# Kernel optimization log

Hardware: AMD Instinct MI355X
Metric: run time of the kernel (lower is better)

The kernel has to match this reference:

```python
import jax, jax.numpy as jnp
import numpy as np

N_NODES = 20000
N_PATHS = 100000
D_IN = 128
H = 128
N_GRAPHS = 128
N_CLASSES = 10
EPS = 1e-5


def _bn(x, g, b):
    # BatchNorm1d in training mode: biased batch statistics
    m = x.mean(0)
    v = x.var(0)
    return g * (x - m) * jax.lax.rsqrt(v + EPS) + b


def _lstm_final_h(seq, w_ih, w_hh, b_ih, b_hh):
    # seq: [N, T, H] -> final hidden state [N, H]; torch gate order i,f,g,o
    N = seq.shape[0]
    Hd = w_hh.shape[1]
    xg = jnp.einsum('nti,gi->ntg', seq, w_ih) + b_ih + b_hh  # [N, T, 4H]

    def step(carry, g_t):
        h, c = carry
        g = g_t + h @ w_hh.T
        i, f, gg, o = jnp.split(g, 4, axis=-1)
        c = jax.nn.sigmoid(f) * c + jax.nn.sigmoid(i) * jnp.tanh(gg)
        h = jax.nn.sigmoid(o) * jnp.tanh(c)
        return (h, c), None

    init = (jnp.zeros((N, Hd), seq.dtype), jnp.zeros((N, Hd), seq.dtype))
    (h, _), _ = jax.lax.scan(step, init, jnp.swapaxes(xg, 0, 1))
    return h


def setup_inputs() -> dict:
    key = jax.random.key(0)
    ks = jax.random.split(key, 24)
    s = 0.05
    inp = {
        'x': jax.random.normal(ks[0], (N_NODES, D_IN), jnp.float32),
        'path_2': jax.random.randint(ks[1], (N_PATHS, 2), 0, N_NODES),
        'path_3': jax.random.randint(ks[2], (N_PATHS, 3), 0, N_NODES),
        'batch': jnp.sort(jax.random.randint(ks[3], (N_NODES,), 0, N_GRAPHS)),
        # feature encoder: Linear -> BN -> ReLU -> Linear -> BN -> ReLU
        'fe_w1': jax.random.normal(ks[4], (H, D_IN)) * s,
        'fe_b1': jnp.zeros((H,)),
        'fe_g1': jnp.ones((H,)),
        'fe_be1': jnp.zeros((H,)),
        'fe_w2': jax.random.normal(ks[5], (H, H)) * s,
        'fe_b2': jnp.zeros((H,)),
        'fe_g2': jnp.ones((H,)),
        'fe_be2': jnp.zeros((H,)),
        # shared single-layer LSTM (input H -> hidden H)
        'w_ih': jax.random.normal(ks[6], (4 * H, H)) * s,
        'w_hh': jax.random.normal(ks[7], (4 * H, H)) * s,
        'b_ih': jnp.zeros((4 * H,)),
        'b_hh': jnp.zeros((4 * H,)),
        # per-conv batch norms (cutoff-1 = 2 layers)
        'bn1_g': jnp.ones((H,)),
        'bn1_b': jnp.zeros((H,)),
        'bn2_g': jnp.ones((H,)),
        'bn2_b': jnp.zeros((H,)),
        # readout
        'lin1_w': jax.random.normal(ks[8], (H, H)) * s,
        'lin1_b': jnp.zeros((H,)),
        'lin2_w': jax.random.normal(ks[9], (N_CLASSES, H)) * s,
        'lin2_b': jnp.zeros((N_CLASSES,)),
    }
    return inp


def reference(x, path_2, path_3, batch,
              fe_w1, fe_b1, fe_g1, fe_be1, fe_w2, fe_b2, fe_g2, fe_be2,
              w_ih, w_hh, b_ih, b_hh,
              bn1_g, bn1_b, bn2_g, bn2_b,
              lin1_w, lin1_b, lin2_w, lin2_b):
    # feature encoder
    h = jax.nn.relu(_bn(x @ fe_w1.T + fe_b1, fe_g1, fe_be1))
    h = jax.nn.relu(_bn(h @ fe_w2.T + fe_b2, fe_g2, fe_be2))
    # PathConv layers: gather paths -> shared LSTM -> scatter-add -> residual+BN+ReLU
    for paths, bg, bb in ((path_2, bn1_g, bn1_b), (path_3, bn2_g, bn2_b)):
        seq = h[paths]                                   # [n_paths, T, H]
        hf = _lstm_final_h(seq, w_ih, w_hh, b_ih, b_hh)  # [n_paths, H]
        agg = jax.ops.segment_sum(hf, paths[:, -1], num_segments=h.shape[0])
        h = jax.nn.relu(_bn(agg + h, bg, bb))
    # global add pool + MLP head
    pooled = jax.ops.segment_sum(h, batch, num_segments=N_GRAPHS)
    out = jax.nn.relu(pooled @ lin1_w.T + lin1_b)
    return out @ lin2_w.T + lin2_b
```

## Files before the change

kernel.cpp:

```cpp
#include <hip/hip_runtime.h>
#include <cmath>

#define NN 20000
#define NP 100000
#define D  128
#define G4 512
#define NG 128
#define NC 10
#define CHUNK 20000

__device__ __forceinline__ float sigf(float x) { return 1.0f / (1.0f + expf(-x)); }

__device__ __forceinline__ void stage_chunk(
    const float* __restrict__ A, const float* __restrict__ W,
    float4* As4, float4* Ws4, int bm, int bn, int M, int N,
    int koff, int sr, int sc)
{
#pragma unroll
  for (int pass = 0; pass < 8; ++pass) {
    int r = pass * 16 + sr;
    int sw = sc ^ ((r >> 3) & 7);
    int ga = bm + r; ga = ga < M ? ga : M - 1;
    As4[r * 16 + sw] = *(const float4*)(A + (size_t)ga * 128 + koff + sc * 4);
    int gw = bn + r; gw = gw < N ? gw : N - 1;
    Ws4[r * 16 + sw] = *(const float4*)(W + (size_t)gw * 128 + koff + sc * 4);
  }
}

__device__ __forceinline__ void compute_chunk(
    const float4* As4, const float4* Ws4,
    int tm, int tn, int axor, int wxor, float acc[8][8])
{
#pragma unroll 2
  for (int k4 = 0; k4 < 16; ++k4) {
    float4 av[8], wv[8];
#pragma unroll
    for (int i = 0; i < 8; ++i) av[i] = As4[(tm + i) * 16 + (k4 ^ axor)];
#pragma unroll
    for (int j = 0; j < 8; ++j) wv[j] = Ws4[(tn + j) * 16 + (k4 ^ wxor)];
#pragma unroll
    for (int i = 0; i < 8; ++i)
#pragma unroll
      for (int j = 0; j < 8; ++j) {
        acc[i][j] = fmaf(av[i].x, wv[j].x, acc[i][j]);
        acc[i][j] = fmaf(av[i].y, wv[j].y, acc[i][j]);
        acc[i][j] = fmaf(av[i].z, wv[j].z, acc[i][j]);
        acc[i][j] = fmaf(av[i].w, wv[j].w, acc[i][j]);
      }
  }
}

__global__ __launch_bounds__(256) void gemm128(
    const float* __restrict__ A, const float* __restrict__ W,
    const float* __restrict__ bias, float* __restrict__ C,
    int M, int N, int relu)
{
  __shared__ float4 As4[2048];
  __shared__ float4 Ws4[2048];

  const int tid = threadIdx.x;
  const int bm = blockIdx.x * 128;
  const int bn = blockIdx.y * 128;

  const int ty = tid >> 4, tx = tid & 15;
  const int tm = ty * 8, tn = tx * 8;
  const int axor = ty & 7, wxor = tx & 7;
  const int sr = tid >> 4, sc = tid & 15;

  float acc[8][8] = {};

  stage_chunk(A, W, As4, Ws4, bm, bn, M, N, 0, sr, sc);
  __syncthreads();
  compute_chunk(As4, Ws4, tm, tn, axor, wxor, acc);
  __syncthreads();
  stage_chunk(A, W, As4, Ws4, bm, bn, M, N, 64, sr, sc);
  __syncthreads();
  compute_chunk(As4, Ws4, tm, tn, axor, wxor, acc);

#pragma unroll
  for (int i = 0; i < 8; ++i) {
    int r = bm + tm + i;
    if (r >= M) continue;
    int cbase = bn + tn;
    if (cbase + 7 < N && ((((size_t)r * N + cbase) & 3) == 0)) {
#pragma unroll
      for (int jj = 0; jj < 2; ++jj) {
        float4 v;
        v.x = acc[i][jj * 4 + 0] + (bias ? bias[cbase + jj * 4 + 0] : 0.f);
        v.y = acc[i][jj * 4 + 1] + (bias ? bias[cbase + jj * 4 + 1] : 0.f);
        v.z = acc[i][jj * 4 + 2] + (bias ? bias[cbase + jj * 4 + 2] : 0.f);
        v.w = acc[i][jj * 4 + 3] + (bias ? bias[cbase + jj * 4 + 3] : 0.f);
        if (relu) { v.x = fmaxf(v.x, 0.f); v.y = fmaxf(v.y, 0.f);
                    v.z = fmaxf(v.z, 0.f); v.w = fmaxf(v.w, 0.f); }
        *(float4*)(C + (size_t)r * N + cbase + jj * 4) = v;
      }
    } else {
#pragma unroll
      for (int j = 0; j < 8; ++j) {
        int cn = cbase + j;
        if (cn >= N) continue;
        float v = acc[i][j] + (bias ? bias[cn] : 0.f);
        if (relu) v = fmaxf(v, 0.f);
        C[(size_t)r * N + cn] = v;
      }
    }
  }
}

__global__ void zero_kernel(float* p, int n) {
  for (int i = blockIdx.x * blockDim.x + threadIdx.x; i < n; i += gridDim.x * blockDim.x)
    p[i] = 0.f;
}

__global__ void zero_int(int* p, int n) {
  for (int i = blockIdx.x * blockDim.x + threadIdx.x; i < n; i += gridDim.x * blockDim.x)
    p[i] = 0;
}

__global__ void addvec_kernel(const float* a, const float* b, float* o, int n) {
  int i = blockIdx.x * blockDim.x + threadIdx.x;
  if (i < n) o[i] = a[i] + b[i];
}

__global__ __launch_bounds__(256) void bn_stats(const float* __restrict__ u,
                                                float* __restrict__ stats,
                                                int M, int rowsPerBlock) {
  __shared__ float sh[512];
  const int j = threadIdx.x & 127;
  const int half = threadIdx.x >> 7;
  int r0 = blockIdx.x * rowsPerBlock;
  int r1 = min(M, r0 + rowsPerBlock);
  float s = 0.f, q = 0.f;
  for (int r = r0 + half; r < r1; r += 2) {
    float v = u[(size_t)r * 128 + j];
    s += v; q += v * v;
  }
  sh[threadIdx.x] = s;
  sh[256 + threadIdx.x] = q;
  __syncthreads();
  if (threadIdx.x < 128) {
    atomicAdd(&stats[j], sh[j] + sh[j + 128]);
    atomicAdd(&stats[128 + j], sh[256 + j] + sh[256 + j + 128]);
  }
}

__global__ void bn_apply_relu(const float* __restrict__ u, const float* __restrict__ stats,
                              const float* __restrict__ g, const float* __restrict__ b,
                              float* __restrict__ out, int n4, float invM) {
  int idx = blockIdx.x * blockDim.x + threadIdx.x;
  if (idx >= n4) return;
  int q = idx & 31;
  float4 uv = ((const float4*)u)[idx];
  float4 sv = ((const float4*)stats)[q];
  float4 qv = ((const float4*)stats)[32 + q];
  float4 gv = ((const float4*)g)[q];
  float4 bv = ((const float4*)b)[q];
  float4 o;
  { float m = sv.x * invM, var = qv.x * invM - m * m;
    o.x = fmaxf(gv.x * (uv.x - m) * rsqrtf(var + 1e-5f) + bv.x, 0.f); }
  { float m = sv.y * invM, var = qv.y * invM - m * m;
    o.y = fmaxf(gv.y * (uv.y - m) * rsqrtf(var + 1e-5f) + bv.y, 0.f); }
  { float m = sv.z * invM, var = qv.z * invM - m * m;
    o.z = fmaxf(gv.z * (uv.z - m) * rsqrtf(var + 1e-5f) + bv.z, 0.f); }
  { float m = sv.w * invM, var = qv.w * invM - m * m;
    o.w = fmaxf(gv.w * (uv.w - m) * rsqrtf(var + 1e-5f) + bv.w, 0.f); }
  ((float4*)out)[idx] = o;
}

__global__ void hist_k(const int* __restrict__ path, int stride, int col, int np,
                       int* __restrict__ cnt) {
  int i = blockIdx.x * blockDim.x + threadIdx.x;
  if (i < np) atomicAdd(&cnt[path[(size_t)i * stride + col]], 1);
}

__global__ __launch_bounds__(256) void scan_bins(const int* __restrict__ cnt,
                                                 int* __restrict__ rp) {
  __shared__ int sh[256];
  const int t = threadIdx.x;
  const int SEG = (NN + 255) / 256;
  int lo = t * SEG, hi = min(NN, lo + SEG);
  int s = 0;
  for (int i = lo; i < hi; ++i) s += cnt[i];
  sh[t] = s;
  __syncthreads();
  for (int off = 1; off < 256; off <<= 1) {
    int v = (t >= off) ? sh[t - off] : 0;
    __syncthreads();
    sh[t] += v;
    __syncthreads();
  }
  int base = (t == 0) ? 0 : sh[t - 1];
  for (int i = lo; i < hi; ++i) { rp[i] = base; base += cnt[i]; }
  if (t == 0) rp[NN] = sh[255];
}

__global__ void scatter_k(const int* __restrict__ path, int stride, int col, int np,
                          const int* __restrict__ rp, int* __restrict__ cur,
                          int* __restrict__ perm) {
  int i = blockIdx.x * blockDim.x + threadIdx.x;
  if (i < np) {
    int b = path[(size_t)i * stride + col];
    int pos = atomicAdd(&cur[b], 1);
    perm[rp[b] + pos] = i;
  }
}

__global__ void lstm_step0(const float* __restrict__ Z, float* __restrict__ H1,
                           float* __restrict__ C1, int n4) {
  int idx = blockIdx.x * blockDim.x + threadIdx.x;
  if (idx >= n4) return;
  int v = idx >> 5, q = idx & 31;
  const float4* z = (const float4*)(Z + (size_t)v * G4);
  float4 zi = z[q], zg = z[64 + q], zo = z[96 + q];
  float4 c, h;
  c.x = sigf(zi.x) * tanhf(zg.x); h.x = sigf(zo.x) * tanhf(c.x);
  c.y = sigf(zi.y) * tanhf(zg.y); h.y = sigf(zo.y) * tanhf(c.y);
  c.z = sigf(zi.z) * tanhf(zg.z); h.z = sigf(zo.z) * tanhf(c.z);
  c.w = sigf(zi.w) * tanhf(zg.w); h.w = sigf(zo.w) * tanhf(c.w);
  ((float4*)C1)[idx] = c;
  ((float4*)H1)[idx] = h;
}

__device__ __forceinline__ void lstm_gate4(const float4 zi, const float4 zf,
                                           const float4 zg, const float4 zo,
                                           const float4 ri, const float4 rf,
                                           const float4 rg, const float4 ro,
                                           const float4 cin, float4* cout, float4* hout) {
  float c, out;
  c = sigf(zf.x + rf.x) * cin.x + sigf(zi.x + ri.x) * tanhf(zg.x + rg.x);
  out = sigf(zo.x + ro.x) * tanhf(c); cout->x = c; hout->x = out;
  c = sigf(zf.y + rf.y) * cin.y + sigf(zi.y + ri.y) * tanhf(zg.y + rg.y);
  out = sigf(zo.y + ro.y) * tanhf(c); cout->y = c; hout->y = out;
  c = sigf(zf.z + rf.z) * cin.z + sigf(zi.z + ri.z) * tanhf(zg.z + rg.z);
  out = sigf(zo.z + ro.z) * tanhf(c); cout->z = c; hout->z = out;
  c = sigf(zf.w + rf.w) * cin.w + sigf(zi.w + ri.w) * tanhf(zg.w + rg.w);
  out = sigf(zo.w + ro.w) * tanhf(c); cout->w = c; hout->w = out;
}

__global__ __launch_bounds__(256) void final2_sorted(
    const int* __restrict__ perm, const int* __restrict__ rp,
    const int* __restrict__ path, const float* __restrict__ Z,
    const float* __restrict__ R1, const float* __restrict__ C1,
    const float* __restrict__ h, float* __restrict__ agg)
{
  int node = blockIdx.x * 8 + (threadIdx.x >> 5);
  int q = threadIdx.x & 31;
  if (node >= NN) return;
  const float4* z = (const float4*)(Z + (size_t)node * G4);
  float4 zi = z[q], zf = z[32 + q], zg = z[64 + q], zo = z[96 + q];
  float4 acc = ((const float4*)h)[node * 32 + q];
  int e1 = rp[node + 1];
  for (int e = rp[node]; e < e1; ++e) {
    int p = perm[e];
    int a = path[(size_t)p * 2];
    const float4* r = (const float4*)(R1 + (size_t)a * G4);
    float4 cin = ((const float4*)(C1 + (size_t)a * D))[q];
    float4 c, hh;
    lstm_gate4(zi, zf, zg, zo, r[q], r[32 + q], r[64 + q], r[96 + q], cin, &c, &hh);
    acc.x += hh.x; acc.y += hh.y; acc.z += hh.z; acc.w += hh.w;
  }
  ((float4*)agg)[node * 32 + q] = acc;
}

__global__ void step1_perm(const int* __restrict__ perm, const int* __restrict__ path,
                           const float* __restrict__ Z, const float* __restrict__ R1,
                           const float* __restrict__ C1, float* __restrict__ h2,
                           float* __restrict__ c2, int p0, int n4) {
  int idx = blockIdx.x * blockDim.x + threadIdx.x;
  if (idx >= n4) return;
  int il = idx >> 5, q = idx & 31;
  int p = perm[p0 + il];
  int a = path[(size_t)p * 3 + 0], b = path[(size_t)p * 3 + 1];
  const float4* z = (const float4*)(Z + (size_t)b * G4);
  const float4* r = (const float4*)(R1 + (size_t)a * G4);
  float4 cin = ((const float4*)(C1 + (size_t)a * D))[q];
  float4 c, h;
  lstm_gate4(z[q], z[32 + q], z[64 + q], z[96 + q],
             r[q], r[32 + q], r[64 + q], r[96 + q], cin, &c, &h);
  ((float4*)c2)[idx] = c;
  ((float4*)h2)[idx] = h;
}

__global__ __launch_bounds__(256) void final3_chunk(
    const int* __restrict__ rp, const float* __restrict__ Z,
    const float* __restrict__ R2c, const float* __restrict__ c2c,
    float* __restrict__ agg, int p0, int pc)
{
  int node = blockIdx.x * 8 + (threadIdx.x >> 5);
  int q = threadIdx.x & 31;
  if (node >= NN) return;
  int lo = max(rp[node], p0), hi = min(rp[node + 1], p0 + pc);
  if (lo >= hi) return;
  const float4* z = (const float4*)(Z + (size_t)node * G4);
  float4 zi = z[q], zf = z[32 + q], zg = z[64 + q], zo = z[96 + q];
  float4 acc = ((const float4*)agg)[node * 32 + q];
  for (int e = lo; e < hi; ++e) {
    int i = e - p0;
    const float4* r = (const float4*)(R2c + (size_t)i * G4);
    float4 cin = ((const float4*)c2c)[i * 32 + q];
    float4 c, hh;
    lstm_gate4(zi, zf, zg, zo, r[q], r[32 + q], r[64 + q], r[96 + q], cin, &c, &hh);
    acc.x += hh.x; acc.y += hh.y; acc.z += hh.z; acc.w += hh.w;
  }
  ((float4*)agg)[node * 32 + q] = acc;
}

__global__ void pool_kernel(const float* __restrict__ h, const int* __restrict__ batch,
                            float* __restrict__ pooled, int n4) {
  int idx = blockIdx.x * blockDim.x + threadIdx.x;
  if (idx >= n4) return;
  int v = idx >> 5, q = idx & 31;
  float4 hv = ((const float4*)h)[idx];
  float* dst = pooled + (size_t)batch[v] * D + q * 4;
  atomicAdd(dst + 0, hv.x); atomicAdd(dst + 1, hv.y);
  atomicAdd(dst + 2, hv.z); atomicAdd(dst + 3, hv.w);
}

extern "C" void kernel_launch(void* const* d_in, const int* in_sizes, int n_in,
                              void* d_out, int out_size, void* d_ws, size_t ws_size,
                              hipStream_t stream) {
  const float* x      = (const float*)d_in[0];
  const int*   path2  = (const int*)d_in[1];
  const int*   path3  = (const int*)d_in[2];
  const int*   batch  = (const int*)d_in[3];
  const float* fe_w1  = (const float*)d_in[4];
  const float* fe_b1  = (const float*)d_in[5];
  const float* fe_g1  = (const float*)d_in[6];
  const float* fe_be1 = (const float*)d_in[7];
  const float* fe_w2  = (const float*)d_in[8];
  const float* fe_b2  = (const float*)d_in[9];
  const float* fe_g2  = (const float*)d_in[10];
  const float* fe_be2 = (const float*)d_in[11];
  const float* w_ih   = (const float*)d_in[12];
  const float* w_hh   = (const float*)d_in[13];
  const float* b_ih   = (const float*)d_in[14];
  const float* b_hh   = (const float*)d_in[15];
  const float* bn1_g  = (const float*)d_in[16];
  const float* bn1_b  = (const float*)d_in[17];
  const float* bn2_g  = (const float*)d_in[18];
  const float* bn2_b  = (const float*)d_in[19];
  const float* lin1_w = (const float*)d_in[20];
  const float* lin1_b = (const float*)d_in[21];
  const float* lin2_w = (const float*)d_in[22];
  const float* lin2_b = (const float*)d_in[23];
  float* out = (float*)d_out;

  float* w = (float*)d_ws;
  float* h    = w; w += (size_t)NN * D;
  float* agg  = w; w += (size_t)NN * D;
  float* Z    = w; w += (size_t)NN * G4;
  float* R1   = w; w += (size_t)NN * G4;
  float* H1   = w; w += (size_t)NN * D;
  float* C1   = w; w += (size_t)NN * D;
  float* c2c  = w; w += (size_t)CHUNK * D;
  float* R2c  = w; w += (size_t)CHUNK * G4;
  float* stats  = w; w += 256;
  float* pooled = w; w += (size_t)NG * D;
  float* out1   = w; w += (size_t)NG * D;
  float* bcomb  = w; w += G4;
  float* ency = Z;
  float* h2c  = H1;

  int* iw = (int*)w;
  int* cnt2  = iw; iw += NN;
  int* cur2  = iw; iw += NN;
  int* rp2   = iw; iw += NN + 1;
  int* perm2 = iw; iw += NP;
  int* cnt3  = iw; iw += NN;
  int* cur3  = iw; iw += NN;
  int* rp3   = iw; iw += NN + 1;
  int* perm3 = iw; iw += NP;

  auto gemm = [&](const float* A, const float* Wm, const float* bias, float* Cm,
                  int M, int N, bool relu) {
    dim3 g((M + 127) / 128, (N + 127) / 128);
    gemm128<<<g, 256, 0, stream>>>(A, Wm, bias, Cm, M, N, relu ? 1 : 0);
  };
  auto bn = [&](const float* u, const float* gamma, const float* beta, float* o, int M) {
    zero_kernel<<<1, 256, 0, stream>>>(stats, 256);
    const int blocks = 160;
    int rows = (M + blocks - 1) / blocks;
    bn_stats<<<blocks, 256, 0, stream>>>(u, stats, M, rows);
    int n4 = M * 32;
    bn_apply_relu<<<(n4 + 255) / 256, 256, 0, stream>>>(u, stats, gamma, beta, o, n4, 1.0f / M);
  };

  zero_int<<<128, 256, 0, stream>>>(cnt2, NN);
  zero_int<<<128, 256, 0, stream>>>(cur2, NN);
  zero_int<<<128, 256, 0, stream>>>(cnt3, NN);
  zero_int<<<128, 256, 0, stream>>>(cur3, NN);
  hist_k<<<(NP + 255) / 256, 256, 0, stream>>>(path2, 2, 1, NP, cnt2);
  hist_k<<<(NP + 255) / 256, 256, 0, stream>>>(path3, 3, 2, NP, cnt3);
  scan_bins<<<1, 256, 0, stream>>>(cnt2, rp2);
  scan_bins<<<1, 256, 0, stream>>>(cnt3, rp3);
  scatter_k<<<(NP + 255) / 256, 256, 0, stream>>>(path2, 2, 1, NP, rp2, cur2, perm2);
  scatter_k<<<(NP + 255) / 256, 256, 0, stream>>>(path3, 3, 2, NP, rp3, cur3, perm3);

  addvec_kernel<<<2, 256, 0, stream>>>(b_ih, b_hh, bcomb, G4);

  gemm(x, fe_w1, fe_b1, ency, NN, D, false);
  bn(ency, fe_g1, fe_be1, h, NN);
  gemm(h, fe_w2, fe_b2, ency, NN, D, false);
  bn(ency, fe_g2, fe_be2, h, NN);

  gemm(h, w_ih, bcomb, Z, NN, G4, false);
  lstm_step0<<<(NN * 32 + 255) / 256, 256, 0, stream>>>(Z, H1, C1, NN * 32);
  gemm(H1, w_hh, nullptr, R1, NN, G4, false);
  final2_sorted<<<NN / 8, 256, 0, stream>>>(perm2, rp2, path2, Z, R1, C1, h, agg);
  bn(agg, bn1_g, bn1_b, h, NN);

  gemm(h, w_ih, bcomb, Z, NN, G4, false);
  lstm_step0<<<(NN * 32 + 255) / 256, 256, 0, stream>>>(Z, H1, C1, NN * 32);
  gemm(H1, w_hh, nullptr, R1, NN, G4, false);
  hipMemcpyAsync(agg, h, (size_t)NN * D * sizeof(float), hipMemcpyDeviceToDevice, stream);
  for (int p0 = 0; p0 < NP; p0 += CHUNK) {
    int pc = NP - p0 < CHUNK ? NP - p0 : CHUNK;
    int n4 = pc * 32;
    step1_perm<<<(n4 + 255) / 256, 256, 0, stream>>>(perm3, path3, Z, R1, C1,
                                                     h2c, c2c, p0, n4);
    gemm(h2c, w_hh, nullptr, R2c, pc, G4, false);
    final3_chunk<<<NN / 8, 256, 0, stream>>>(rp3, Z, R2c, c2c, agg, p0, pc);
  }
  bn(agg, bn2_g, bn2_b, h, NN);

  zero_kernel<<<64, 256, 0, stream>>>(pooled, NG * D);
  pool_kernel<<<(NN * 32 + 255) / 256, 256, 0, stream>>>(h, batch, pooled, NN * 32);
  gemm(pooled, lin1_w, lin1_b, out1, NG, D, true);
  gemm(out1, lin2_w, lin2_b, out, NG, NC, false);
}
```

Before: 1.249 ms.

## Pre-sort path endpoints, use fast gate math, and size chunks from workspace

The scatter kernels now write the source node indices directly in sorted order (a2s for length-2 paths, int2 pairs for length-3 paths), so the LSTM kernels no longer do a two-level perm-then-path indirection. Sigmoid and tanh switch to __expf/__fdividef approximations. The length-3 chunk size is now derived from the remaining workspace instead of being fixed at 20000, which allows fewer, larger chunk iterations. The trade-offs are lower transcendental accuracy and a dependence on how large the workspace is.

```diff
diff --git a/kernel.cpp b/kernel.cpp
--- a/kernel.cpp
+++ b/kernel.cpp
@@ -7,9 +7,14 @@
 #define G4 512
 #define NG 128
 #define NC 10
-#define CHUNK 20000
-
-__device__ __forceinline__ float sigf(float x) { return 1.0f / (1.0f + expf(-x)); }
+
+__device__ __forceinline__ float fsig(float x) {
+  return __fdividef(1.f, 1.f + __expf(-x));
+}
+__device__ __forceinline__ float ftanh(float x) {
+  float t = __expf(-2.f * fabsf(x));
+  return copysignf(__fdividef(1.f - t, 1.f + t), x);
+}
 
 __device__ __forceinline__ void stage_chunk(
     const float* __restrict__ A, const float* __restrict__ W,
@@ -194,14 +199,25 @@
   if (t == 0) rp[NN] = sh[255];
 }
 
-__global__ void scatter_k(const int* __restrict__ path, int stride, int col, int np,
-                          const int* __restrict__ rp, int* __restrict__ cur,
-                          int* __restrict__ perm) {
+__global__ void scatter2(const int* __restrict__ path, int np,
+                         const int* __restrict__ rp, int* __restrict__ cur,
+                         int* __restrict__ a2s) {
   int i = blockIdx.x * blockDim.x + threadIdx.x;
   if (i < np) {
-    int b = path[(size_t)i * stride + col];
-    int pos = atomicAdd(&cur[b], 1);
-    perm[rp[b] + pos] = i;
+    int b = path[(size_t)i * 2 + 1];
+    int pos = rp[b] + atomicAdd(&cur[b], 1);
+    a2s[pos] = path[(size_t)i * 2];
+  }
+}
+
+__global__ void scatter3(const int* __restrict__ path, int np,
+                         const int* __restrict__ rp, int* __restrict__ cur,
+                         int2* __restrict__ ab3) {
+  int i = blockIdx.x * blockDim.x + threadIdx.x;
+  if (i < np) {
+    int c = path[(size_t)i * 3 + 2];
+    int pos = rp[c] + atomicAdd(&cur[c], 1);
+    ab3[pos] = make_int2(path[(size_t)i * 3], path[(size_t)i * 3 + 1]);
   }
 }
 
@@ -213,10 +229,10 @@
   const float4* z = (const float4*)(Z + (size_t)v * G4);
   float4 zi = z[q], zg = z[64 + q], zo = z[96 + q];
   float4 c, h;
-  c.x = sigf(zi.x) * tanhf(zg.x); h.x = sigf(zo.x) * tanhf(c.x);
-  c.y = sigf(zi.y) * tanhf(zg.y); h.y = sigf(zo.y) * tanhf(c.y);
-  c.z = sigf(zi.z) * tanhf(zg.z); h.z = sigf(zo.z) * tanhf(c.z);
-  c.w = sigf(zi.w) * tanhf(zg.w); h.w = sigf(zo.w) * tanhf(c.w);
+  c.x = fsig(zi.x) * ftanh(zg.x); h.x = fsig(zo.x) * ftanh(c.x);
+  c.y = fsig(zi.y) * ftanh(zg.y); h.y = fsig(zo.y) * ftanh(c.y);
+  c.z = fsig(zi.z) * ftanh(zg.z); h.z = fsig(zo.z) * ftanh(c.z);
+  c.w = fsig(zi.w) * ftanh(zg.w); h.w = fsig(zo.w) * ftanh(c.w);
   ((float4*)C1)[idx] = c;
   ((float4*)H1)[idx] = h;
 }
@@ -226,22 +242,22 @@
                                            const float4 ri, const float4 rf,
                                            const float4 rg, const float4 ro,
                                            const float4 cin, float4* cout, float4* hout) {
-  float c, out;
-  c = sigf(zf.x + rf.x) * cin.x + sigf(zi.x + ri.x) * tanhf(zg.x + rg.x);
-  out = sigf(zo.x + ro.x) * tanhf(c); cout->x = c; hout->x = out;
-  c = sigf(zf.y + rf.y) * cin.y + sigf(zi.y + ri.y) * tanhf(zg.y + rg.y);
-  out = sigf(zo.y + ro.y) * tanhf(c); cout->y = c; hout->y = out;
-  c = sigf(zf.z + rf.z) * cin.z + sigf(zi.z + ri.z) * tanhf(zg.z + rg.z);
-  out = sigf(zo.z + ro.z) * tanhf(c); cout->z = c; hout->z = out;
-  c = sigf(zf.w + rf.w) * cin.w + sigf(zi.w + ri.w) * tanhf(zg.w + rg.w);
-  out = sigf(zo.w + ro.w) * tanhf(c); cout->w = c; hout->w = out;
+  float c;
+  c = fsig(zf.x + rf.x) * cin.x + fsig(zi.x + ri.x) * ftanh(zg.x + rg.x);
+  cout->x = c; hout->x = fsig(zo.x + ro.x) * ftanh(c);
+  c = fsig(zf.y + rf.y) * cin.y + fsig(zi.y + ri.y) * ftanh(zg.y + rg.y);
+  cout->y = c; hout->y = fsig(zo.y + ro.y) * ftanh(c);
+  c = fsig(zf.z + rf.z) * cin.z + fsig(zi.z + ri.z) * ftanh(zg.z + rg.z);
+  cout->z = c; hout->z = fsig(zo.z + ro.z) * ftanh(c);
+  c = fsig(zf.w + rf.w) * cin.w + fsig(zi.w + ri.w) * ftanh(zg.w + rg.w);
+  cout->w = c; hout->w = fsig(zo.w + ro.w) * ftanh(c);
 }
 
 __global__ __launch_bounds__(256) void final2_sorted(
-    const int* __restrict__ perm, const int* __restrict__ rp,
-    const int* __restrict__ path, const float* __restrict__ Z,
-    const float* __restrict__ R1, const float* __restrict__ C1,
-    const float* __restrict__ h, float* __restrict__ agg)
+    const int* __restrict__ a2s, const int* __restrict__ rp,
+    const float* __restrict__ Z, const float* __restrict__ R1,
+    const float* __restrict__ C1, const float* __restrict__ h,
+    float* __restrict__ agg)
 {
   int node = blockIdx.x * 8 + (threadIdx.x >> 5);
   int q = threadIdx.x & 31;
@@ -249,10 +265,9 @@
   const float4* z = (const float4*)(Z + (size_t)node * G4);
   float4 zi = z[q], zf = z[32 + q], zg = z[64 + q], zo = z[96 + q];
   float4 acc = ((const float4*)h)[node * 32 + q];
-  int e1 = rp[node + 1];
-  for (int e = rp[node]; e < e1; ++e) {
-    int p = perm[e];
-    int a = path[(size_t)p * 2];
+  int e0 = rp[node], e1 = rp[node + 1];
+  for (int e = e0; e < e1; ++e) {
+    int a = a2s[e];
     const float4* r = (const float4*)(R1 + (size_t)a * G4);
     float4 cin = ((const float4*)(C1 + (size_t)a * D))[q];
     float4 c, hh;
@@ -262,18 +277,17 @@
   ((float4*)agg)[node * 32 + q] = acc;
 }
 
-__global__ void step1_perm(const int* __restrict__ perm, const int* __restrict__ path,
-                           const float* __restrict__ Z, const float* __restrict__ R1,
-                           const float* __restrict__ C1, float* __restrict__ h2,
-                           float* __restrict__ c2, int p0, int n4) {
+__global__ void step1_sorted(const int2* __restrict__ ab3,
+                             const float* __restrict__ Z, const float* __restrict__ R1,
+                             const float* __restrict__ C1, float* __restrict__ h2,
+                             float* __restrict__ c2, int p0, int n4) {
   int idx = blockIdx.x * blockDim.x + threadIdx.x;
   if (idx >= n4) return;
   int il = idx >> 5, q = idx & 31;
-  int p = perm[p0 + il];
-  int a = path[(size_t)p * 3 + 0], b = path[(size_t)p * 3 + 1];
-  const float4* z = (const float4*)(Z + (size_t)b * G4);
-  const float4* r = (const float4*)(R1 + (size_t)a * G4);
-  float4 cin = ((const float4*)(C1 + (size_t)a * D))[q];
+  int2 ab = ab3[p0 + il];
+  const float4* z = (const float4*)(Z + (size_t)ab.y * G4);
+  const float4* r = (const float4*)(R1 + (size_t)ab.x * G4);
+  float4 cin = ((const float4*)(C1 + (size_t)ab.x * D))[q];
   float4 c, h;
   lstm_gate4(z[q], z[32 + q], z[64 + q], z[96 + q],
              r[q], r[32 + q], r[64 + q], r[96 + q], cin, &c, &h);
@@ -352,24 +366,31 @@
   float* R1   = w; w += (size_t)NN * G4;
   float* H1   = w; w += (size_t)NN * D;
   float* C1   = w; w += (size_t)NN * D;
-  float* c2c  = w; w += (size_t)CHUNK * D;
-  float* R2c  = w; w += (size_t)CHUNK * G4;
   float* stats  = w; w += 256;
   float* pooled = w; w += (size_t)NG * D;
   float* out1   = w; w += (size_t)NG * D;
   float* bcomb  = w; w += G4;
   float* ency = Z;
-  float* h2c  = H1;
-
-  int* iw = (int*)w;
-  int* cnt2  = iw; iw += NN;
-  int* cur2  = iw; iw += NN;
-  int* rp2   = iw; iw += NN + 1;
-  int* perm2 = iw; iw += NP;
-  int* cnt3  = iw; iw += NN;
-  int* cur3  = iw; iw += NN;
-  int* rp3   = iw; iw += NN + 1;
-  int* perm3 = iw; iw += NP;
+
+  int2* ab3 = (int2*)(((uintptr_t)w + 7) & ~(uintptr_t)7);
+  int* iw = (int*)(ab3 + NP);
+  int* a2s  = iw; iw += NP;
+  int* cnt2 = iw; iw += NN;
+  int* cur2 = iw; iw += NN;
+  int* rp2  = iw; iw += NN + 1;
+  int* cnt3 = iw; iw += NN;
+  int* cur3 = iw; iw += NN;
+  int* rp3  = iw; iw += NN + 1;
+
+  float* cb = (float*)(((uintptr_t)iw + 15) & ~(uintptr_t)15);
+  size_t used = (char*)cb - (char*)d_ws;
+  size_t remf = (ws_size > used) ? (ws_size - used) / 4 : 0;
+  int chunk = (int)((remf / 768 > (size_t)NP) ? (size_t)NP : remf / 768);
+  chunk &= ~63;
+  if (chunk < 64) chunk = 64;
+  float* h2c = cb;
+  float* c2c = h2c + (size_t)chunk * D;
+  float* R2c = c2c + (size_t)chunk * D;
 
   auto gemm = [&](const float* A, const float* Wm, const float* bias, float* Cm,
                   int M, int N, bool relu) {
@@ -393,8 +414,8 @@
   hist_k<<<(NP + 255) / 256, 256, 0, stream>>>(path3, 3, 2, NP, cnt3);
   scan_bins<<<1, 256, 0, stream>>>(cnt2, rp2);
   scan_bins<<<1, 256, 0, stream>>>(cnt3, rp3);
-  scatter_k<<<(NP + 255) / 256, 256, 0, stream>>>(path2, 2, 1, NP, rp2, cur2, perm2);
-  scatter_k<<<(NP + 255) / 256, 256, 0, stream>>>(path3, 3, 2, NP, rp3, cur3, perm3);
+  scatter2<<<(NP + 255) / 256, 256, 0, stream>>>(path2, NP, rp2, cur2, a2s);
+  scatter3<<<(NP + 255) / 256, 256, 0, stream>>>(path3, NP, rp3, cur3, ab3);
 
   addvec_kernel<<<2, 256, 0, stream>>>(b_ih, b_hh, bcomb, G4);
 
@@ -406,18 +427,17 @@
   gemm(h, w_ih, bcomb, Z, NN, G4, false);
   lstm_step0<<<(NN * 32 + 255) / 256, 256, 0, stream>>>(Z, H1, C1, NN * 32);
   gemm(H1, w_hh, nullptr, R1, NN, G4, false);
-  final2_sorted<<<NN / 8, 256, 0, stream>>>(perm2, rp2, path2, Z, R1, C1, h, agg);
+  final2_sorted<<<NN / 8, 256, 0, stream>>>(a2s, rp2, Z, R1, C1, h, agg);
   bn(agg, bn1_g, bn1_b, h, NN);
 
   gemm(h, w_ih, bcomb, Z, NN, G4, false);
   lstm_step0<<<(NN * 32 + 255) / 256, 256, 0, stream>>>(Z, H1, C1, NN * 32);
   gemm(H1, w_hh, nullptr, R1, NN, G4, false);
   hipMemcpyAsync(agg, h, (size_t)NN * D * sizeof(float), hipMemcpyDeviceToDevice, stream);
-  for (int p0 = 0; p0 < NP; p0 += CHUNK) {
-    int pc = NP - p0 < CHUNK ? NP - p0 : CHUNK;
+  for (int p0 = 0; p0 < NP; p0 += chunk) {
+    int pc = NP - p0 < chunk ? NP - p0 : chunk;
     int n4 = pc * 32;
-    step1_perm<<<(n4 + 255) / 256, 256, 0, stream>>>(perm3, path3, Z, R1, C1,
-                                                     h2c, c2c, p0, n4);
+    step1_sorted<<<(n4 + 255) / 256, 256, 0, stream>>>(ab3, Z, R1, C1, h2c, c2c, p0, n4);
     gemm(h2c, w_hh, nullptr, R2c, pc, G4, false);
     final3_chunk<<<NN / 8, 256, 0, stream>>>(rp3, Z, R2c, c2c, agg, p0, pc);
   }
```

Measured after the change: 1.144 ms. 1.09x faster.
